# Kernel optimization log

Hardware: AMD Instinct MI355X
Metric: run time of the kernel (lower is better)

The kernel has to match this reference:

```python
import jax, jax.numpy as jnp
import numpy as np

HIDDEN = 1024
NUM_HEADS = 16
HEAD_DIM = HIDDEN // NUM_HEADS


def rotate_half(x):
    x1, x2 = jnp.split(x, 2, axis=-1)
    return jnp.concatenate((-x2, x1), axis=-1)


def rope_tables(T, dim, dtype):
    inv_freq = 1.0 / (10000.0 ** (jnp.arange(0, dim, 2, dtype=jnp.float32) / dim))
    t = jnp.arange(T, dtype=jnp.float32)
    freqs = t[:, None] * inv_freq[None, :]           # [T, dim/2]
    emb = jnp.concatenate((freqs, freqs), axis=-1)   # [T, dim]
    return jnp.cos(emb).astype(dtype), jnp.sin(emb).astype(dtype)


def setup_inputs() -> dict:
    key = jax.random.key(0)
    kx, kq, kk, kv, ko = jax.random.split(key, 5)
    B, T = 2, 2048
    scale = 1.0 / np.sqrt(HIDDEN)
    return {
        "x": jax.random.normal(kx, (B, T, HIDDEN), dtype=jnp.float32),
        "wq": jax.random.normal(kq, (HIDDEN, HIDDEN), dtype=jnp.float32) * scale,
        "wk": jax.random.normal(kk, (HIDDEN, HIDDEN), dtype=jnp.float32) * scale,
        "wv": jax.random.normal(kv, (HIDDEN, HIDDEN), dtype=jnp.float32) * scale,
        "wo": jax.random.normal(ko, (HIDDEN, HIDDEN), dtype=jnp.float32) * scale,
    }


def reference(x, wq, wk, wv, wo):
    B, T, _ = x.shape
    H, D = NUM_HEADS, HEAD_DIM
    # projections (Linear, no bias): x @ W.T; reshape to [B, H, T, D]
    q = (x @ wq.T).reshape(B, T, H, D).transpose(0, 2, 1, 3)
    k = (x @ wk.T).reshape(B, T, H, D).transpose(0, 2, 1, 3)
    v = (x @ wv.T).reshape(B, T, H, D).transpose(0, 2, 1, 3)
    cos, sin = rope_tables(T, D, x.dtype)            # [T, D]
    cos = cos[None, None]                            # [1,1,T,D]
    sin = sin[None, None]
    q = q * cos + rotate_half(q) * sin
    k = k * cos + rotate_half(k) * sin
    scores = jnp.einsum("bhtd,bhsd->bhts", q, k) / np.sqrt(D).astype(x.dtype)
    attn = jax.nn.softmax(scores, axis=-1)
    out = jnp.einsum("bhts,bhsd->bhtd", attn, v)     # [B,H,T,D]
    out = out.transpose(0, 2, 1, 3).reshape(B, T, H * D)
    return out @ wo.T
```

## Files before the change

### kernel.cpp

```cpp
#include <hip/hip_runtime.h>
#include <hip/hip_bf16.h>
#include <stdint.h>

typedef __bf16 bf16;
typedef __attribute__((ext_vector_type(8))) __bf16 bf16x8;
typedef __attribute__((ext_vector_type(4))) float f32x4;
typedef __attribute__((ext_vector_type(16))) float f32x16;

#define L2E 1.4426950408889634f

__device__ __forceinline__ f32x4 mfma16(bf16x8 a, bf16x8 b, f32x4 c) {
  return __builtin_amdgcn_mfma_f32_16x16x32_bf16(a, b, c, 0, 0, 0);
}

__device__ __forceinline__ f32x16 mfma32(bf16x8 a, bf16x8 b, f32x16 c) {
  return __builtin_amdgcn_mfma_f32_32x32x16_bf16(a, b, c, 0, 0, 0);
}

__device__ __forceinline__ void gload16(void* lds, const void* g) {
  __builtin_amdgcn_global_load_lds(
      (const __attribute__((address_space(1))) uint32_t*)g,
      (__attribute__((address_space(3))) uint32_t*)lds, 16, 0, 0);
}

__device__ __forceinline__ unsigned cvt_pk_bf16(float lo, float hi) {
  unsigned r;
  asm("v_cvt_pk_bf16_f32 %0, %1, %2" : "=v"(r) : "v"(lo), "v"(hi));
  return r;
}

__device__ __forceinline__ void pl32swap(unsigned& a, unsigned& b) {
  auto r = __builtin_amdgcn_permlane32_swap(a, b, false, false);
  a = r[0];
  b = r[1];
}

__global__ __launch_bounds__(256) void prep_cast(
    const float* __restrict__ x, const float* __restrict__ wq,
    const float* __restrict__ wk, const float* __restrict__ wv,
    const float* __restrict__ wo, bf16* __restrict__ xb,
    bf16* __restrict__ wqb, bf16* __restrict__ wkb, bf16* __restrict__ wvb,
    bf16* __restrict__ wob, float* __restrict__ ct, float* __restrict__ st) {
  int blk = blockIdx.x;
  if (blk >= 8192) {
    int i = (blk - 8192) * 256 + threadIdx.x;
    int t = i >> 5, d = i & 31;
    float inv = powf(10000.f, -(float)d * (1.f / 32.f));
    float a = (float)t * inv;
    ct[i] = cosf(a);
    st[i] = sinf(a);
    return;
  }
  int i = blk * 256 + threadIdx.x;
  const int NX = 4096 * 1024 / 4;
  const int NW = 1024 * 1024 / 4;
  const float* src; bf16* dst; int off;
  if (i < NX)               { src = x;  dst = xb;  off = i; }
  else if (i < NX + NW)     { src = wq; dst = wqb; off = i - NX; }
  else if (i < NX + 2 * NW) { src = wk; dst = wkb; off = i - (NX + NW); }
  else if (i < NX + 3 * NW) { src = wv; dst = wvb; off = i - (NX + 2 * NW); }
  else                      { src = wo; dst = wob; off = i - (NX + 3 * NW); }
  float4 v = ((const float4*)src)[off];
  union { bf16 h[4]; uint2 u; } o;
  o.h[0] = (bf16)v.x; o.h[1] = (bf16)v.y; o.h[2] = (bf16)v.z; o.h[3] = (bf16)v.w;
  ((uint2*)dst)[off] = o.u;
}

__device__ __forceinline__ void gemm_mainloop(const bf16* __restrict__ A,
                                              const bf16* __restrict__ W,
                                              int m0, int n0,
                                              bf16 (*As)[4096], bf16 (*Bs)[4096],
                                              f32x4 acc[4][4]) {
  const int tid = threadIdx.x;
  const int lane = tid & 63, wave = tid >> 6;
  const int wr = (wave >> 1) * 64, wc = (wave & 1) * 64;
  const int lr = lane & 15, lh = lane >> 4;

  auto stage = [&](bf16* dA, bf16* dB, int kt) {
    int k0 = kt * 32;
#pragma unroll
    for (int p = 0; p < 2; p++) {
      int u = p * 256 + tid; int row = u >> 2; int kg = (u & 3) ^ (row & 3);
      gload16(dA + (size_t)u * 8, A + (size_t)(m0 + row) * 1024 + k0 + kg * 8);
    }
#pragma unroll
    for (int p = 0; p < 2; p++) {
      int u = p * 256 + tid; int row = u >> 2; int kg = (u & 3) ^ (row & 3);
      gload16(dB + (size_t)u * 8, W + (size_t)(n0 + row) * 1024 + k0 + kg * 8);
    }
  };

  stage(As[0], Bs[0], 0);
  int cur = 0;
  for (int kt = 0; kt < 32; ++kt) {
    __syncthreads();
    const bf16* cA = As[cur]; const bf16* cB = Bs[cur];
    bf16x8 af[4], bfr[4];
#pragma unroll
    for (int i = 0; i < 4; i++) {
      int row = wr + i * 16 + lr; int un = row * 4 + (lh ^ (row & 3));
      af[i] = *(const bf16x8*)(cA + (size_t)un * 8);
    }
#pragma unroll
    for (int j = 0; j < 4; j++) {
      int row = wc + j * 16 + lr; int un = row * 4 + (lh ^ (row & 3));
      bfr[j] = *(const bf16x8*)(cB + (size_t)un * 8);
    }
    if (kt + 1 < 32) stage(As[cur ^ 1], Bs[cur ^ 1], kt + 1);
#pragma unroll
    for (int i = 0; i < 4; i++)
#pragma unroll
      for (int j = 0; j < 4; j++) acc[i][j] = mfma16(af[i], bfr[j], acc[i][j]);
    cur ^= 1;
  }
}

__global__ __launch_bounds__(256) void gemm_qkv(
    const bf16* __restrict__ xb, const bf16* __restrict__ wq,
    const bf16* __restrict__ wk, const bf16* __restrict__ wv,
    const float* __restrict__ ct, const float* __restrict__ st,
    bf16* __restrict__ qo, bf16* __restrict__ ko, bf16* __restrict__ vto) {
  __shared__ __align__(16) bf16 As[2][4096];
  __shared__ __align__(16) bf16 Bs[2][4096];
  int bm = blockIdx.x, bn = blockIdx.y;
  int proj = bn >> 3;
  const bf16* W = proj == 0 ? wq : (proj == 1 ? wk : wv);
  int m0 = bm * 128, n0 = (bn & 7) * 128;

  f32x4 zero = {0.f, 0.f, 0.f, 0.f};
  f32x4 acc[4][4];
#pragma unroll
  for (int i = 0; i < 4; i++)
#pragma unroll
    for (int j = 0; j < 4; j++) acc[i][j] = zero;

  gemm_mainloop(xb, W, m0, n0, As, Bs, acc);

  const int tid = threadIdx.x, lane = tid & 63, wave = tid >> 6;
  const int wr = (wave >> 1) * 64, wc = (wave & 1) * 64;
  const int lr = lane & 15, lh = lane >> 4;

  if (proj == 2) {
#pragma unroll
    for (int i = 0; i < 4; i++) {
      int t0 = m0 + wr + i * 16 + lh * 4;
      int b = t0 >> 11, tt = t0 & 2047;
#pragma unroll
      for (int j = 0; j < 4; j++) {
        int col = n0 + wc + j * 16 + lr;
        int h = col >> 6, d = col & 63;
        union { bf16 h4[4]; uint2 u; } pk4;
#pragma unroll
        for (int r = 0; r < 4; r++) pk4.h4[r] = (bf16)acc[i][j][r];
        *(uint2*)(vto + ((size_t)(b * 16 + h) * 64 + d) * 2048 + tt) = pk4.u;
      }
    }
    return;
  }

  bf16* out = proj == 0 ? qo : ko;
  int colb = n0 + wc;
  int h = colb >> 6;
  const float QSC = 0.125f * L2E;
#pragma unroll
  for (int i = 0; i < 4; i++) {
#pragma unroll
    for (int r = 0; r < 4; r++) {
      int m = m0 + wr + i * 16 + lh * 4 + r;
      int b = m >> 11, t = m & 2047;
      float v0 = acc[i][0][r], v1 = acc[i][1][r];
      float v2 = acc[i][2][r], v3 = acc[i][3][r];
      {
        float c0 = ct[t * 32 + lr],      s0 = st[t * 32 + lr];
        float c1 = ct[t * 32 + 16 + lr], s1 = st[t * 32 + 16 + lr];
        float n0v = v0 * c0 - v2 * s0, n2 = v2 * c0 + v0 * s0;
        float n1 = v1 * c1 - v3 * s1,  n3 = v3 * c1 + v1 * s1;
        v0 = n0v; v1 = n1; v2 = n2; v3 = n3;
        if (proj == 0) { v0 *= QSC; v1 *= QSC; v2 *= QSC; v3 *= QSC; }
      }
      size_t base = ((size_t)(b * 16 + h) * 2048 + t) * 64;
      out[base + lr]      = (bf16)v0;
      out[base + 16 + lr] = (bf16)v1;
      out[base + 32 + lr] = (bf16)v2;
      out[base + 48 + lr] = (bf16)v3;
    }
  }
}

__global__ __launch_bounds__(256, 2) void attn(const bf16* __restrict__ q,
                                               const bf16* __restrict__ k,
                                               const bf16* __restrict__ vt,
                                               bf16* __restrict__ o) {
  __shared__ __align__(16) char smb[49152];
  int pidx = blockIdx.x;
  int L = (pidx & 7) * 64 + (pidx >> 3);
  int bh = L >> 4, qt = L & 15;

  const int tid = threadIdx.x, lane = tid & 63, wave = tid >> 6;
  const int lq = lane & 31, hi = lane >> 5;
  const int sub = wave & 1;
  const int c = wave >> 1;

  const bf16* kg = k + (size_t)bh * 131072;
  const bf16* vg = vt + (size_t)bh * 131072;

  int q0 = qt * 128 + sub * 64;
  const bf16* qbp = q + ((size_t)bh * 2048 + q0) * 64;
  bf16x8 qf[2][4];
#pragma unroll
  for (int qb = 0; qb < 2; qb++)
#pragma unroll
    for (int kk = 0; kk < 4; kk++)
      qf[qb][kk] =
          *(const bf16x8*)(qbp + (size_t)(qb * 32 + lq) * 64 + kk * 16 + hi * 8);

  int vaK[4];
  {
    int rowK = c * 32 + lq;
#pragma unroll
    for (int kk = 0; kk < 4; kk++)
      vaK[kk] = rowK * 128 + (((2 * kk + hi) ^ (rowK & 7)) << 4);
  }
  int vaV[2][2];
#pragma unroll
  for (int cc = 0; cc < 2; cc++)
#pragma unroll
    for (int db = 0; db < 2; db++)
      vaV[cc][db] = 8192 + (db * 32 + lq) * 128 +
                    (((4 * c + 2 * cc + hi) ^ (lq & 7)) << 4);

  int kofe[2], vofe[2], ldsK[2], ldsV[2];
#pragma unroll
  for (int pp = 0; pp < 2; pp++) {
    int uu = pp * 256 + tid;
    int r = uu >> 3, lu = uu & 7, su = lu ^ (r & 7);
    kofe[pp] = r * 64 + su * 8;
    vofe[pp] = r * 2048 + su * 8;
    ldsK[pp] = uu * 16;
    ldsV[pp] = 8192 + uu * 16;
  }

  f32x16 acc[2][2];
  f32x16 CM;
#pragma unroll
  for (int r = 0; r < 16; r++) {
    acc[0][0][r] = 0.f; acc[0][1][r] = 0.f;
    acc[1][0][r] = 0.f; acc[1][1][r] = 0.f;
    CM[r] = -16.f;
  }
  float l0 = 0.f, l1 = 0.f;

  auto stage = [&](int bo, int t) {
#pragma unroll
    for (int pp = 0; pp < 2; pp++) {
      gload16(smb + bo + ldsK[pp], kg + t * 4096 + kofe[pp]);
      gload16(smb + bo + ldsV[pp], vg + t * 64 + vofe[pp]);
    }
  };

  auto compute = [&](int bo) {
    bf16x8 ka[4], vv[2][2];
#pragma unroll
    for (int kk = 0; kk < 4; kk++)
      ka[kk] = *(const bf16x8*)(smb + bo + vaK[kk]);
#pragma unroll
    for (int cc = 0; cc < 2; cc++)
#pragma unroll
      for (int db = 0; db < 2; db++)
        vv[cc][db] = *(const bf16x8*)(smb + bo + vaV[cc][db]);

    __builtin_amdgcn_s_setprio(1);
    f32x16 s0 = mfma32(ka[0], qf[0][0], CM);
    f32x16 s1 = mfma32(ka[0], qf[1][0], CM);
#pragma unroll
    for (int kk = 1; kk < 4; kk++) {
      s0 = mfma32(ka[kk], qf[0][kk], s0);
      s1 = mfma32(ka[kk], qf[1][kk], s1);
    }
    __builtin_amdgcn_s_setprio(0);

    unsigned pk0[8], pk1[8];
    {
      float sa = 0.f, sb = 0.f;
#pragma unroll
      for (int i = 0; i < 8; i++) {
        float pa = __builtin_amdgcn_exp2f(s0[2 * i]);
        float pb = __builtin_amdgcn_exp2f(s0[2 * i + 1]);
        sa += pa; sb += pb;
        pk0[i] = cvt_pk_bf16(pa, pb);
      }
      l0 += sa + sb;
    }
    {
      float sa = 0.f, sb = 0.f;
#pragma unroll
      for (int i = 0; i < 8; i++) {
        float pa = __builtin_amdgcn_exp2f(s1[2 * i]);
        float pb = __builtin_amdgcn_exp2f(s1[2 * i + 1]);
        sa += pa; sb += pb;
        pk1[i] = cvt_pk_bf16(pa, pb);
      }
      l1 += sa + sb;
    }

    pl32swap(pk0[0], pk0[2]); pl32swap(pk0[1], pk0[3]);
    pl32swap(pk0[4], pk0[6]); pl32swap(pk0[5], pk0[7]);
    pl32swap(pk1[0], pk1[2]); pl32swap(pk1[1], pk1[3]);
    pl32swap(pk1[4], pk1[6]); pl32swap(pk1[5], pk1[7]);

    __builtin_amdgcn_s_setprio(1);
#pragma unroll
    for (int cc = 0; cc < 2; cc++) {
      union { unsigned u[4]; bf16x8 v; } pb0, pb1;
#pragma unroll
      for (int w = 0; w < 4; w++) {
        pb0.u[w] = pk0[4 * cc + w];
        pb1.u[w] = pk1[4 * cc + w];
      }
#pragma unroll
      for (int db = 0; db < 2; db++) {
        acc[0][db] = mfma32(vv[cc][db], pb0.v, acc[0][db]);
        acc[1][db] = mfma32(vv[cc][db], pb1.v, acc[1][db]);
      }
    }
    __builtin_amdgcn_s_setprio(0);
  };

  stage(0, 0);
  stage(16384, 1);
  int boC = 0, boS = 32768;
  for (int t = 0; t < 31; ++t) {
    asm volatile("s_waitcnt vmcnt(4)" ::: "memory");
    __builtin_amdgcn_s_barrier();
    if (t + 2 < 32) stage(boS, t + 2);
    compute(boC);
    boC += 16384; if (boC == 49152) boC = 0;
    boS += 16384; if (boS == 49152) boS = 0;
  }
  asm volatile("s_waitcnt vmcnt(0)" ::: "memory");
  __builtin_amdgcn_s_barrier();
  compute(boC);

  __syncthreads();
  float* abuf = (float*)smb;
  float* lbuf = (float*)(smb + 32768);
  if (c == 1) {
#pragma unroll
    for (int qb = 0; qb < 2; qb++)
#pragma unroll
      for (int db = 0; db < 2; db++)
#pragma unroll
        for (int r = 0; r < 16; r++)
          abuf[((sub * 4 + qb * 2 + db) * 16 + r) * 64 + lane] = acc[qb][db][r];
    lbuf[(sub * 2 + 0) * 64 + lane] = l0;
    lbuf[(sub * 2 + 1) * 64 + lane] = l1;
  }
  __syncthreads();
  if (c == 1) return;
#pragma unroll
  for (int qb = 0; qb < 2; qb++)
#pragma unroll
    for (int db = 0; db < 2; db++)
#pragma unroll
      for (int r = 0; r < 16; r++)
        acc[qb][db][r] += abuf[((sub * 4 + qb * 2 + db) * 16 + r) * 64 + lane];
  l0 += lbuf[(sub * 2 + 0) * 64 + lane];
  l1 += lbuf[(sub * 2 + 1) * 64 + lane];

  {
    unsigned ta = __float_as_uint(l0), tb = ta;
    pl32swap(ta, tb);
    l0 = __uint_as_float(ta) + __uint_as_float(tb);
  }
  {
    unsigned ta = __float_as_uint(l1), tb = ta;
    pl32swap(ta, tb);
    l1 = __uint_as_float(ta) + __uint_as_float(tb);
  }
  float inv[2] = {1.0f / l0, 1.0f / l1};
  int b = bh >> 4, h = bh & 15;
#pragma unroll
  for (int qb = 0; qb < 2; qb++) {
    int qrow = q0 + qb * 32 + lq;
    bf16* orow = o + ((size_t)(b * 2048 + qrow)) * 1024 + h * 64;
#pragma unroll
    for (int db = 0; db < 2; db++)
#pragma unroll
      for (int g = 0; g < 4; g++) {
        union { bf16 h4[4]; uint2 u; } t;
#pragma unroll
        for (int e = 0; e < 4; e++)
          t.h4[e] = (bf16)(acc[qb][db][4 * g + e] * inv[qb]);
        *(uint2*)(orow + db * 32 + 8 * g + 4 * hi) = t.u;
      }
  }
}

__global__ __launch_bounds__(256) void gemm_out(const bf16* __restrict__ ab,
                                                const bf16* __restrict__ wo,
                                                float* __restrict__ out) {
  __shared__ __align__(16) bf16 As[2][4096];
  __shared__ __align__(16) bf16 Bs[2][4096];
  int m0 = blockIdx.x * 128, n0 = blockIdx.y * 128;
  f32x4 zero = {0.f, 0.f, 0.f, 0.f};
  f32x4 acc[4][4];
#pragma unroll
  for (int i = 0; i < 4; i++)
#pragma unroll
    for (int j = 0; j < 4; j++) acc[i][j] = zero;

  gemm_mainloop(ab, wo, m0, n0, As, Bs, acc);

  const int tid = threadIdx.x, lane = tid & 63, wave = tid >> 6;
  const int wr = (wave >> 1) * 64, wc = (wave & 1) * 64;
  const int lr = lane & 15, lh = lane >> 4;
#pragma unroll
  for (int i = 0; i < 4; i++)
#pragma unroll
    for (int r = 0; r < 4; r++) {
      int m = m0 + wr + i * 16 + lh * 4 + r;
#pragma unroll
      for (int j = 0; j < 4; j++) {
        int col = n0 + wc + j * 16 + lr;
        out[(size_t)m * 1024 + col] = acc[i][j][r];
      }
    }
}

extern "C" void kernel_launch(void* const* d_in, const int* in_sizes, int n_in,
                              void* d_out, int out_size, void* d_ws, size_t ws_size,
                              hipStream_t stream) {
  const float* x  = (const float*)d_in[0];
  const float* wq = (const float*)d_in[1];
  const float* wk = (const float*)d_in[2];
  const float* wv = (const float*)d_in[3];
  const float* wo = (const float*)d_in[4];
  float* out = (float*)d_out;
  char* ws = (char*)d_ws;
  const size_t MB = 1u << 20;
  bf16* xb  = (bf16*)(ws + 0);
  bf16* wqb = (bf16*)(ws + 8 * MB);
  bf16* wkb = (bf16*)(ws + 10 * MB);
  bf16* wvb = (bf16*)(ws + 12 * MB);
  bf16* wob = (bf16*)(ws + 14 * MB);
  bf16* qw  = (bf16*)(ws + 16 * MB);
  bf16* kw  = (bf16*)(ws + 24 * MB);
  bf16* vtw = (bf16*)(ws + 32 * MB);
  bf16* aw  = (bf16*)(ws + 40 * MB);
  float* ct = (float*)(ws + 48 * MB);
  float* st = (float*)(ws + 48 * MB + 256 * 1024);

  prep_cast<<<8448, 256, 0, stream>>>(x, wq, wk, wv, wo, xb, wqb, wkb, wvb,
                                      wob, ct, st);
  gemm_qkv<<<dim3(32, 24), 256, 0, stream>>>(xb, wqb, wkb, wvb, ct, st, qw, kw,
                                             vtw);
  attn<<<512, 256, 0, stream>>>(qw, kw, vtw, aw);
  gemm_out<<<dim3(32, 8), 256, 0, stream>>>(aw, wob, out);
}
```

Measured before the change: 116.4 us.

## Halve attention query tile per block, double grid, and use double-buffered LDS

The attention kernel now gives each block 64 query rows instead of 128, so each wave holds one 32-row Q fragment instead of two and the grid doubles to 1024 blocks. The K/V pipeline goes from a triple-buffered vmcnt-based prefetch to a double-buffered loop with a __syncthreads per tile, which cuts LDS to 32KB and raises the launch-bounds occupancy target to 4 blocks per CU. The aim is more concurrent waves and lower register pressure to hide latency. In exchange every K/V tile is loaded from memory twice as often per query row, and the simpler pipeline adds a full barrier per iteration.

```diff
diff --git a/kernel.cpp b/kernel.cpp
--- a/kernel.cpp
+++ b/kernel.cpp
@@ -187,14 +187,14 @@
   }
 }
 
-__global__ __launch_bounds__(256, 2) void attn(const bf16* __restrict__ q,
+__global__ __launch_bounds__(256, 4) void attn(const bf16* __restrict__ q,
                                                const bf16* __restrict__ k,
                                                const bf16* __restrict__ vt,
                                                bf16* __restrict__ o) {
-  __shared__ __align__(16) char smb[49152];
+  __shared__ __align__(16) char smb[32768];
   int pidx = blockIdx.x;
-  int L = (pidx & 7) * 64 + (pidx >> 3);
-  int bh = L >> 4, qt = L & 15;
+  int L = (pidx & 7) * 128 + (pidx >> 3);
+  int bh = L >> 5, qt = L & 31;
 
   const int tid = threadIdx.x, lane = tid & 63, wave = tid >> 6;
   const int lq = lane & 31, hi = lane >> 5;
@@ -204,15 +204,12 @@
   const bf16* kg = k + (size_t)bh * 131072;
   const bf16* vg = vt + (size_t)bh * 131072;
 
-  int q0 = qt * 128 + sub * 64;
+  int q0 = qt * 64 + sub * 32;
   const bf16* qbp = q + ((size_t)bh * 2048 + q0) * 64;
-  bf16x8 qf[2][4];
-#pragma unroll
-  for (int qb = 0; qb < 2; qb++)
-#pragma unroll
-    for (int kk = 0; kk < 4; kk++)
-      qf[qb][kk] =
-          *(const bf16x8*)(qbp + (size_t)(qb * 32 + lq) * 64 + kk * 16 + hi * 8);
+  bf16x8 qf[4];
+#pragma unroll
+  for (int kk = 0; kk < 4; kk++)
+    qf[kk] = *(const bf16x8*)(qbp + (size_t)lq * 64 + kk * 16 + hi * 8);
 
   int vaK[4];
   {
@@ -240,15 +237,14 @@
     ldsV[pp] = 8192 + uu * 16;
   }
 
-  f32x16 acc[2][2];
+  f32x16 acc[2];
   f32x16 CM;
 #pragma unroll
   for (int r = 0; r < 16; r++) {
-    acc[0][0][r] = 0.f; acc[0][1][r] = 0.f;
-    acc[1][0][r] = 0.f; acc[1][1][r] = 0.f;
+    acc[0][r] = 0.f; acc[1][r] = 0.f;
     CM[r] = -16.f;
   }
-  float l0 = 0.f, l1 = 0.f;
+  float l0 = 0.f;
 
   auto stage = [&](int bo, int t) {
 #pragma unroll
@@ -270,16 +266,12 @@
         vv[cc][db] = *(const bf16x8*)(smb + bo + vaV[cc][db]);
 
     __builtin_amdgcn_s_setprio(1);
-    f32x16 s0 = mfma32(ka[0], qf[0][0], CM);
-    f32x16 s1 = mfma32(ka[0], qf[1][0], CM);
-#pragma unroll
-    for (int kk = 1; kk < 4; kk++) {
-      s0 = mfma32(ka[kk], qf[0][kk], s0);
-      s1 = mfma32(ka[kk], qf[1][kk], s1);
-    }
+    f32x16 s0 = mfma32(ka[0], qf[0], CM);
+#pragma unroll
+    for (int kk = 1; kk < 4; kk++) s0 = mfma32(ka[kk], qf[kk], s0);
     __builtin_amdgcn_s_setprio(0);
 
-    unsigned pk0[8], pk1[8];
+    unsigned pk0[8];
     {
       float sa = 0.f, sb = 0.f;
 #pragma unroll
@@ -291,109 +283,68 @@
       }
       l0 += sa + sb;
     }
-    {
-      float sa = 0.f, sb = 0.f;
-#pragma unroll
-      for (int i = 0; i < 8; i++) {
-        float pa = __builtin_amdgcn_exp2f(s1[2 * i]);
-        float pb = __builtin_amdgcn_exp2f(s1[2 * i + 1]);
-        sa += pa; sb += pb;
-        pk1[i] = cvt_pk_bf16(pa, pb);
-      }
-      l1 += sa + sb;
-    }
 
     pl32swap(pk0[0], pk0[2]); pl32swap(pk0[1], pk0[3]);
     pl32swap(pk0[4], pk0[6]); pl32swap(pk0[5], pk0[7]);
-    pl32swap(pk1[0], pk1[2]); pl32swap(pk1[1], pk1[3]);
-    pl32swap(pk1[4], pk1[6]); pl32swap(pk1[5], pk1[7]);
 
     __builtin_amdgcn_s_setprio(1);
 #pragma unroll
     for (int cc = 0; cc < 2; cc++) {
-      union { unsigned u[4]; bf16x8 v; } pb0, pb1;
-#pragma unroll
-      for (int w = 0; w < 4; w++) {
-        pb0.u[w] = pk0[4 * cc + w];
-        pb1.u[w] = pk1[4 * cc + w];
-      }
-#pragma unroll
-      for (int db = 0; db < 2; db++) {
-        acc[0][db] = mfma32(vv[cc][db], pb0.v, acc[0][db]);
-        acc[1][db] = mfma32(vv[cc][db], pb1.v, acc[1][db]);
-      }
+      union { unsigned u[4]; bf16x8 v; } pb0;
+#pragma unroll
+      for (int w = 0; w < 4; w++) pb0.u[w] = pk0[4 * cc + w];
+#pragma unroll
+      for (int db = 0; db < 2; db++)
+        acc[db] = mfma32(vv[cc][db], pb0.v, acc[db]);
     }
     __builtin_amdgcn_s_setprio(0);
   };
 
   stage(0, 0);
-  stage(16384, 1);
-  int boC = 0, boS = 32768;
-  for (int t = 0; t < 31; ++t) {
-    asm volatile("s_waitcnt vmcnt(4)" ::: "memory");
-    __builtin_amdgcn_s_barrier();
-    if (t + 2 < 32) stage(boS, t + 2);
-    compute(boC);
-    boC += 16384; if (boC == 49152) boC = 0;
-    boS += 16384; if (boS == 49152) boS = 0;
-  }
-  asm volatile("s_waitcnt vmcnt(0)" ::: "memory");
-  __builtin_amdgcn_s_barrier();
-  compute(boC);
-
   __syncthreads();
+  for (int t = 0; t < 32; ++t) {
+    if (t + 1 < 32) stage(((t & 1) ^ 1) * 16384, t + 1);
+    compute((t & 1) * 16384);
+    __syncthreads();
+  }
+
   float* abuf = (float*)smb;
-  float* lbuf = (float*)(smb + 32768);
+  float* lbuf = (float*)(smb + 16384);
   if (c == 1) {
 #pragma unroll
-    for (int qb = 0; qb < 2; qb++)
-#pragma unroll
-      for (int db = 0; db < 2; db++)
-#pragma unroll
-        for (int r = 0; r < 16; r++)
-          abuf[((sub * 4 + qb * 2 + db) * 16 + r) * 64 + lane] = acc[qb][db][r];
-    lbuf[(sub * 2 + 0) * 64 + lane] = l0;
-    lbuf[(sub * 2 + 1) * 64 + lane] = l1;
+    for (int db = 0; db < 2; db++)
+#pragma unroll
+      for (int r = 0; r < 16; r++)
+        abuf[((sub * 2 + db) * 16 + r) * 64 + lane] = acc[db][r];
+    lbuf[sub * 64 + lane] = l0;
   }
   __syncthreads();
   if (c == 1) return;
 #pragma unroll
-  for (int qb = 0; qb < 2; qb++)
-#pragma unroll
-    for (int db = 0; db < 2; db++)
-#pragma unroll
-      for (int r = 0; r < 16; r++)
-        acc[qb][db][r] += abuf[((sub * 4 + qb * 2 + db) * 16 + r) * 64 + lane];
-  l0 += lbuf[(sub * 2 + 0) * 64 + lane];
-  l1 += lbuf[(sub * 2 + 1) * 64 + lane];
+  for (int db = 0; db < 2; db++)
+#pragma unroll
+    for (int r = 0; r < 16; r++)
+      acc[db][r] += abuf[((sub * 2 + db) * 16 + r) * 64 + lane];
+  l0 += lbuf[sub * 64 + lane];
 
   {
     unsigned ta = __float_as_uint(l0), tb = ta;
     pl32swap(ta, tb);
     l0 = __uint_as_float(ta) + __uint_as_float(tb);
   }
-  {
-    unsigned ta = __float_as_uint(l1), tb = ta;
-    pl32swap(ta, tb);
-    l1 = __uint_as_float(ta) + __uint_as_float(tb);
-  }
-  float inv[2] = {1.0f / l0, 1.0f / l1};
+  float inv = 1.0f / l0;
   int b = bh >> 4, h = bh & 15;
-#pragma unroll
-  for (int qb = 0; qb < 2; qb++) {
-    int qrow = q0 + qb * 32 + lq;
-    bf16* orow = o + ((size_t)(b * 2048 + qrow)) * 1024 + h * 64;
-#pragma unroll
-    for (int db = 0; db < 2; db++)
-#pragma unroll
-      for (int g = 0; g < 4; g++) {
-        union { bf16 h4[4]; uint2 u; } t;
-#pragma unroll
-        for (int e = 0; e < 4; e++)
-          t.h4[e] = (bf16)(acc[qb][db][4 * g + e] * inv[qb]);
-        *(uint2*)(orow + db * 32 + 8 * g + 4 * hi) = t.u;
-      }
-  }
+  int qrow = q0 + lq;
+  bf16* orow = o + ((size_t)(b * 2048 + qrow)) * 1024 + h * 64;
+#pragma unroll
+  for (int db = 0; db < 2; db++)
+#pragma unroll
+    for (int g = 0; g < 4; g++) {
+      union { bf16 h4[4]; uint2 u; } t;
+#pragma unroll
+      for (int e = 0; e < 4; e++) t.h4[e] = (bf16)(acc[db][4 * g + e] * inv);
+      *(uint2*)(orow + db * 32 + 8 * g + 4 * hi) = t.u;
+    }
 }
 
 __global__ __launch_bounds__(256) void gemm_out(const bf16* __restrict__ ab,
@@ -454,6 +405,6 @@
                                       wob, ct, st);
   gemm_qkv<<<dim3(32, 24), 256, 0, stream>>>(xb, wqb, wkb, wvb, ct, st, qw, kw,
                                              vtw);
-  attn<<<512, 256, 0, stream>>>(qw, kw, vtw, aw);
+  attn<<<1024, 256, 0, stream>>>(qw, kw, vtw, aw);
   gemm_out<<<dim3(32, 8), 256, 0, stream>>>(aw, wob, out);
 }
```

After: 133.5 us. +14.6%, slower.
